# Performance work log

Hardware: AMD Instinct MI355X
Metric: run time of the kernel (lower is better)

The kernel has to match this reference:

```python
import jax, jax.numpy as jnp
import numpy as np

EPS = 1e-5  # torch BatchNorm1d default eps
N, E, F, H, P = 50000, 640000, 128, 128, 64


def batch_norm(h):
    # track_running_stats=False, affine=False -> per-batch mean / biased var
    mu = jnp.mean(h, axis=0)
    var = jnp.mean((h - mu) ** 2, axis=0)
    return (h - mu) * jax.lax.rsqrt(var + EPS)


def gcn_conv(x, src, dst, W, b, n_nodes):
    # GCNConv: D^{-1/2} (A + I) D^{-1/2} X W + b
    h = x @ W
    loop = jnp.arange(n_nodes)
    s = jnp.concatenate([src, loop])
    d = jnp.concatenate([dst, loop])
    deg = jax.ops.segment_sum(jnp.ones(s.shape[0], h.dtype), d, num_segments=n_nodes)
    inv_sqrt = jax.lax.rsqrt(jnp.maximum(deg, 1.0))  # deg >= 1 due to self loops
    msg = h[s] * (inv_sqrt[s] * inv_sqrt[d])[:, None]  # [E+N, H]
    return jax.ops.segment_sum(msg, d, num_segments=n_nodes) + b


def setup_inputs() -> dict:
    key = jax.random.key(0)
    ks = jax.random.split(key, 12)
    s = 0.05
    return {
        "x": jax.random.normal(ks[0], (N, F), jnp.float32),
        "core_values": jax.random.uniform(ks[1], (N,), jnp.float32),
        "W0": jax.random.normal(ks[2], (F, H), jnp.float32) * s,
        "b0": jnp.zeros((H,), jnp.float32),
        "W1": jax.random.normal(ks[3], (H, H), jnp.float32) * s,
        "b1": jnp.zeros((H,), jnp.float32),
        "lin1_W": jax.random.normal(ks[4], (3 * H, H), jnp.float32) * s,
        "lin1_b": jnp.zeros((H,), jnp.float32),
        "lin2_W": jax.random.normal(ks[5], (H, 1), jnp.float32) * s,
        "lin2_b": jnp.zeros((1,), jnp.float32),
        "edge_index": jax.random.randint(ks[6], (2, E), 0, N, jnp.int64 if jax.config.read("jax_enable_x64") else jnp.int32),
        "part_id": jax.random.randint(ks[7], (N,), 0, P, jnp.int32),
        "curr_node_id": 123,
        "num_partitions": P,
    }


def reference(x, core_values, W0, b0, W1, b1, lin1_W, lin1_b, lin2_W, lin2_b,
              edge_index, part_id, curr_node_id, num_partitions):
    n_nodes = x.shape[0]
    src, dst = edge_index[0], edge_index[1]

    # GNN stack: conv -> batchnorm -> relu (num_layers = 2)
    for W, b in ((W0, b0), (W1, b1)):
        x = jax.nn.relu(batch_norm(gcn_conv(x, src, dst, W, b, n_nodes)))

    # getPartitonEmbedding_usingCoreValue as fused segment reductions
    cv = core_values[:, None]
    core = jax.ops.segment_sum(x * cv, part_id, num_segments=num_partitions)
    non_core = jax.ops.segment_sum(x * (1.0 - cv), part_id, num_segments=num_partitions)
    partition_embedding = jnp.concatenate([core, non_core], axis=1)  # [P, 2H]

    x_curr = jnp.broadcast_to(x[curr_node_id][None, :], (num_partitions, x.shape[1]))
    z = jnp.concatenate([x_curr, partition_embedding], axis=1)  # [P, 3H]
    z = jax.nn.relu(z @ lin1_W + lin1_b)
    return z @ lin2_W + lin2_b  # [P, 1]
```

## Files before the change

kernel.cpp:

```cpp
#include <hip/hip_runtime.h>
#include <math.h>

#define EPSV 1e-5f
#define PSORT_NB 256
#define SCAN_NB 256

typedef __attribute__((ext_vector_type(8))) short bf16x8;
typedef __attribute__((ext_vector_type(4))) float f32x4;

__device__ __forceinline__ uint f2b(float f) {
  uint u = __builtin_bit_cast(uint, f);
  return (u + 0x7FFFu + ((u >> 16) & 1u)) >> 16;
}
__device__ __forceinline__ float blo(uint v) { return __builtin_bit_cast(float, v << 16); }
__device__ __forceinline__ float bhi(uint v) { return __builtin_bit_cast(float, v & 0xFFFF0000u); }
__device__ __forceinline__ float b2f(ushort u) { return __builtin_bit_cast(float, ((uint)u) << 16); }

__global__ __launch_bounds__(256) void k_pre1(int* __restrict__ hist, int nbZero,
                                              const int* __restrict__ part,
                                              int* __restrict__ blockHist,
                                              const float* __restrict__ W0,
                                              const float* __restrict__ W1,
                                              ushort* __restrict__ WT0,
                                              ushort* __restrict__ WT1, int n) {
  const int b = blockIdx.x, tid = threadIdx.x;
  if (b < nbZero) {
    int i = b * 256 + tid;
    if (i < n) hist[i] = 0;
  } else if (b < nbZero + PSORT_NB) {
    __shared__ int lh[64];
    int pb = b - nbZero;
    if (tid < 64) lh[tid] = 0;
    __syncthreads();
    int chunk = (n + PSORT_NB - 1) / PSORT_NB;
    int beg = pb * chunk, end = min(n, beg + chunk);
    for (int i = beg + tid; i < end; i += 256) atomicAdd(&lh[part[i]], 1);
    __syncthreads();
    if (tid < 64) blockHist[pb * 64 + tid] = lh[tid];
  } else {
    int idx = (b - nbZero - PSORT_NB) * 256 + tid;
    const float* W = (idx < 16384) ? W0 : W1;
    ushort* WT = (idx < 16384) ? WT0 : WT1;
    int j = idx & 16383;
    int c = j >> 7, k = j & 127;
    WT[j] = (ushort)f2b(W[k * 128 + c]);
  }
}

__global__ __launch_bounds__(256) void k_pre2(const int* __restrict__ dst,
                                              int* __restrict__ hist,
                                              int* __restrict__ rank, int e, int eb,
                                              const int* __restrict__ blockHist,
                                              int* __restrict__ base,
                                              int* __restrict__ ptot) {
  const int b = blockIdx.x, tid = threadIdx.x;
  if (b < eb) {
    int i = b * 256 + tid;
    if (i < e) rank[i] = atomicAdd(&hist[dst[i]], 1);
  } else {
    __shared__ int wtot[4];
    const int p = b - eb;
    const int lane = tid & 63, w = tid >> 6;
    int v = blockHist[tid * 64 + p];
    int x = v;
    #pragma unroll
    for (int off = 1; off < 64; off <<= 1) {
      int y = __shfl_up(x, off);
      if (lane >= off) x += y;
    }
    if (lane == 63) wtot[w] = x;
    __syncthreads();
    int woff = 0;
    if (w > 0) woff = wtot[0];
    if (w > 1) woff += wtot[1];
    if (w > 2) woff += wtot[2];
    base[tid * 64 + p] = woff + x - v;
    if (tid == 255) ptot[p] = woff + x;
  }
}

__global__ __launch_bounds__(256) void k_pre3(const int* __restrict__ hist,
                                              int* __restrict__ row_start,
                                              float* __restrict__ invs,
                                              int* __restrict__ bsum, int n,
                                              const int* __restrict__ ptot,
                                              int* __restrict__ pexcl,
                                              int* __restrict__ pstart) {
  const int b = blockIdx.x, tid = threadIdx.x;
  if (b < SCAN_NB) {
    __shared__ int wtot[4];
    __shared__ int tot;
    const int lane = tid & 63, w = tid >> 6;
    const int chunk = (n + SCAN_NB - 1) / SCAN_NB;
    const int beg = b * chunk, end = min(n, beg + chunk);
    int running = 0;
    for (int t0 = beg; t0 < end; t0 += 256) {
      int i = t0 + tid;
      int v = (i < end) ? hist[i] : 0;
      int x = v;
      #pragma unroll
      for (int off = 1; off < 64; off <<= 1) {
        int y = __shfl_up(x, off);
        if (lane >= off) x += y;
      }
      if (lane == 63) wtot[w] = x;
      __syncthreads();
      if (tid == 0) {
        int a0 = wtot[0], a1 = wtot[1], a2 = wtot[2], a3 = wtot[3];
        wtot[0] = 0; wtot[1] = a0; wtot[2] = a0 + a1; wtot[3] = a0 + a1 + a2;
        tot = a0 + a1 + a2 + a3;
      }
      __syncthreads();
      if (i < end) {
        row_start[i] = running + wtot[w] + x - v;
        invs[i] = rsqrtf((float)(v + 1));
      }
      running += tot;
      __syncthreads();
    }
    if (tid == 0) bsum[b] = running;
  } else if (tid < 64) {
    int v = ptot[tid];
    int x = v;
    #pragma unroll
    for (int off = 1; off < 64; off <<= 1) {
      int y = __shfl_up(x, off);
      if (tid >= off) x += y;
    }
    int excl = x - v;
    pexcl[tid] = excl;
    pstart[tid] = excl;
    if (tid == 63) pstart[64] = x;
  }
}

__global__ __launch_bounds__(256) void k_pre4(const int* __restrict__ bsum,
                                              int* __restrict__ boff,
                                              int* __restrict__ row_start, int n,
                                              const int* __restrict__ part,
                                              const int* __restrict__ base,
                                              const int* __restrict__ pexcl,
                                              int* __restrict__ perm) {
  const int b = blockIdx.x, tid = threadIdx.x;
  if (b == 0) {
    if (tid < 64) {
      int v0 = bsum[tid * 4], v1 = bsum[tid * 4 + 1], v2 = bsum[tid * 4 + 2], v3 = bsum[tid * 4 + 3];
      int s = v0 + v1 + v2 + v3;
      int x = s;
      #pragma unroll
      for (int off = 1; off < 64; off <<= 1) {
        int y = __shfl_up(x, off);
        if (tid >= off) x += y;
      }
      int run = x - s;
      boff[tid * 4] = run; run += v0;
      boff[tid * 4 + 1] = run; run += v1;
      boff[tid * 4 + 2] = run; run += v2;
      boff[tid * 4 + 3] = run;
      if (tid == 63) row_start[n] = x;
    }
  } else {
    __shared__ int cur[64];
    const int pb = b - 1;
    if (tid < 64) cur[tid] = base[pb * 64 + tid] + pexcl[tid];
    __syncthreads();
    int chunk = (n + PSORT_NB - 1) / PSORT_NB;
    int beg = pb * chunk, end = min(n, beg + chunk);
    for (int i = beg + tid; i < end; i += 256) {
      int pos = atomicAdd(&cur[part[i]], 1);
      perm[pos] = i;
    }
  }
}

__global__ __launch_bounds__(256) void k_scan3(int* __restrict__ row_start,
                                               const int* __restrict__ boff, int n) {
  const int b = blockIdx.x, tid = threadIdx.x;
  const int chunk = (n + SCAN_NB - 1) / SCAN_NB;
  const int beg = b * chunk, end = min(n, beg + chunk);
  const int off = boff[b];
  for (int i = beg + tid; i < end; i += 256) row_start[i] += off;
}

__global__ __launch_bounds__(256) void k_scatter(const int* __restrict__ src,
                                                 const int* __restrict__ dst,
                                                 const int* __restrict__ rank,
                                                 const int* __restrict__ row_start,
                                                 int* __restrict__ csr, int e) {
  int i = blockIdx.x * 256 + threadIdx.x;
  if (i < e) csr[row_start[dst[i]] + rank[i]] = src[i];
}

template <bool BN>
__global__ __launch_bounds__(256) void k_gemm(const void* __restrict__ inp,
                                              const ushort* __restrict__ WT,
                                              const float* __restrict__ invs,
                                              const float* __restrict__ stats_red,
                                              ushort* __restrict__ outb, int n) {
  __shared__ ushort As[16384];
  __shared__ ushort Bs[16384];
  __shared__ float muL[128], sclL[128];
  const int tid = threadIdx.x;
  const int l = tid & 63, w = tid >> 6;
  const int br0 = blockIdx.x * 128;

  if (BN) {
    if (tid < 128) {
      float s = stats_red[tid], q = stats_red[128 + tid];
      float m = s * (1.0f / 50000.0f);
      muL[tid] = m;
      sclL[tid] = rsqrtf(q * (1.0f / 50000.0f) - m * m + EPSV);
    }
    __syncthreads();
  }

  #pragma unroll
  for (int i = 0; i < 8; ++i) {
    int flat = i * 2048 + tid * 8;
    int c = flat >> 7;
    uint4 v = *(const uint4*)&WT[flat];
    *(uint4*)&Bs[flat ^ ((c & 7) << 3)] = v;
  }
  #pragma unroll
  for (int i = 0; i < 8; ++i) {
    int flat = i * 2048 + tid * 8;
    int row = flat >> 7, k0 = flat & 127;
    int grow = br0 + row;
    uint4 u;
    if (grow < n) {
      if (BN) {
        const ushort* inb = (const ushort*)inp;
        uint4 raw = *(const uint4*)&inb[(size_t)grow * 128 + k0];
        float f[8] = {blo(raw.x), bhi(raw.x), blo(raw.y), bhi(raw.y),
                      blo(raw.z), bhi(raw.z), blo(raw.w), bhi(raw.w)};
        #pragma unroll
        for (int j = 0; j < 8; ++j) {
          float v = (f[j] - muL[k0 + j]) * sclL[k0 + j];
          f[j] = v > 0.f ? v : 0.f;
        }
        u.x = f2b(f[0]) | (f2b(f[1]) << 16);
        u.y = f2b(f[2]) | (f2b(f[3]) << 16);
        u.z = f2b(f[4]) | (f2b(f[5]) << 16);
        u.w = f2b(f[6]) | (f2b(f[7]) << 16);
      } else {
        const float* inf = (const float*)inp;
        float4 v0 = *(const float4*)&inf[(size_t)grow * 128 + k0];
        float4 v1 = *(const float4*)&inf[(size_t)grow * 128 + k0 + 4];
        u.x = f2b(v0.x) | (f2b(v0.y) << 16);
        u.y = f2b(v0.z) | (f2b(v0.w) << 16);
        u.z = f2b(v1.x) | (f2b(v1.y) << 16);
        u.w = f2b(v1.z) | (f2b(v1.w) << 16);
      }
    } else {
      u.x = u.y = u.z = u.w = 0u;
    }
    *(uint4*)&As[flat ^ ((row & 7) << 3)] = u;
  }
  __syncthreads();

  const int wr = w >> 1, wc = w & 1;
  const int lr = l & 15, lk = (l >> 4) * 8;
  f32x4 acc[4][4];
  #pragma unroll
  for (int m = 0; m < 4; ++m)
    #pragma unroll
    for (int nn = 0; nn < 4; ++nn) acc[m][nn] = (f32x4){0.f, 0.f, 0.f, 0.f};

  #pragma unroll
  for (int ks = 0; ks < 4; ++ks) {
    bf16x8 af[4], bfr[4];
    #pragma unroll
    for (int m = 0; m < 4; ++m) {
      int row = wr * 64 + m * 16 + lr;
      af[m] = *(const bf16x8*)&As[(row * 128 + ks * 32 + lk) ^ ((row & 7) << 3)];
    }
    #pragma unroll
    for (int nn = 0; nn < 4; ++nn) {
      int c = wc * 64 + nn * 16 + lr;
      bfr[nn] = *(const bf16x8*)&Bs[(c * 128 + ks * 32 + lk) ^ ((c & 7) << 3)];
    }
    #pragma unroll
    for (int m = 0; m < 4; ++m)
      #pragma unroll
      for (int nn = 0; nn < 4; ++nn)
        acc[m][nn] = __builtin_amdgcn_mfma_f32_16x16x32_bf16(af[m], bfr[nn], acc[m][nn], 0, 0, 0);
  }

  #pragma unroll
  for (int m = 0; m < 4; ++m) {
    #pragma unroll
    for (int r = 0; r < 4; ++r) {
      int row = br0 + wr * 64 + m * 16 + (l >> 4) * 4 + r;
      if (row >= n) continue;
      float iv = invs[row];
      #pragma unroll
      for (int nn = 0; nn < 4; ++nn) {
        int col = wc * 64 + nn * 16 + lr;
        outb[(size_t)row * 128 + col] = (ushort)f2b(acc[m][nn][r] * iv);
      }
    }
  }
}

__global__ __launch_bounds__(256) void k_gather(const ushort* __restrict__ hsb,
                                                const int* __restrict__ row_start,
                                                const int* __restrict__ csr,
                                                const float* __restrict__ invs,
                                                const float* __restrict__ bias,
                                                ushort* __restrict__ outb,
                                                float* __restrict__ statsP, int n) {
  const int tid = threadIdx.x;
  const int lane = tid & 63, w = tid >> 6;
  const int c0 = lane * 2;
  const ushort* hc = hsb + c0;
  float s0 = 0.f, s1 = 0.f, q0 = 0.f, q1 = 0.f;
  const float bv0 = bias[c0], bv1 = bias[c0 + 1];
  const int stride = gridDim.x * 4;
  for (int node = blockIdx.x * 4 + w; node < n; node += stride) {
    uint vs = *(const uint*)&hc[(size_t)node * 128];
    float accx = blo(vs), accy = bhi(vs);
    int beg = row_start[node], end = row_start[node + 1];
    int e = beg;
    for (; e + 7 < end; e += 8) {
      int sA = csr[e], sB = csr[e + 1], sC = csr[e + 2], sD = csr[e + 3];
      int sE = csr[e + 4], sF = csr[e + 5], sG = csr[e + 6], sH = csr[e + 7];
      uint vA = *(const uint*)&hc[(size_t)sA * 128];
      uint vB = *(const uint*)&hc[(size_t)sB * 128];
      uint vC = *(const uint*)&hc[(size_t)sC * 128];
      uint vD = *(const uint*)&hc[(size_t)sD * 128];
      uint vE = *(const uint*)&hc[(size_t)sE * 128];
      uint vF = *(const uint*)&hc[(size_t)sF * 128];
      uint vG = *(const uint*)&hc[(size_t)sG * 128];
      uint vH = *(const uint*)&hc[(size_t)sH * 128];
      accx += ((blo(vA) + blo(vB)) + (blo(vC) + blo(vD))) +
              ((blo(vE) + blo(vF)) + (blo(vG) + blo(vH)));
      accy += ((bhi(vA) + bhi(vB)) + (bhi(vC) + bhi(vD))) +
              ((bhi(vE) + bhi(vF)) + (bhi(vG) + bhi(vH)));
    }
    for (; e + 3 < end; e += 4) {
      int sA = csr[e], sB = csr[e + 1], sC = csr[e + 2], sD = csr[e + 3];
      uint vA = *(const uint*)&hc[(size_t)sA * 128];
      uint vB = *(const uint*)&hc[(size_t)sB * 128];
      uint vC = *(const uint*)&hc[(size_t)sC * 128];
      uint vD = *(const uint*)&hc[(size_t)sD * 128];
      accx += (blo(vA) + blo(vB)) + (blo(vC) + blo(vD));
      accy += (bhi(vA) + bhi(vB)) + (bhi(vC) + bhi(vD));
    }
    for (; e < end; ++e) {
      uint vA = *(const uint*)&hc[(size_t)csr[e] * 128];
      accx += blo(vA);
      accy += bhi(vA);
    }
    float iv = invs[node];
    float o0 = accx * iv + bv0, o1 = accy * iv + bv1;
    *(uint*)&outb[(size_t)node * 128 + c0] = f2b(o0) | (f2b(o1) << 16);
    s0 += o0; s1 += o1; q0 += o0 * o0; q1 += o1 * o1;
  }
  __shared__ float redS[4][128], redQ[4][128];
  redS[w][c0] = s0; redS[w][c0 + 1] = s1;
  redQ[w][c0] = q0; redQ[w][c0 + 1] = q1;
  __syncthreads();
  if (tid < 128) {
    float s = redS[0][tid] + redS[1][tid] + redS[2][tid] + redS[3][tid];
    statsP[blockIdx.x * 256 + tid] = s;
  } else {
    int t = tid - 128;
    float q = redQ[0][t] + redQ[1][t] + redQ[2][t] + redQ[3][t];
    statsP[blockIdx.x * 256 + tid] = q;
  }
}

__global__ __launch_bounds__(1024) void k_finstats(const float* __restrict__ statsP,
                                                   float* __restrict__ stats_red,
                                                   int nb) {
  int t = threadIdx.x;
  int c = blockIdx.x * 16 + (t & 15);
  int b0 = t >> 4;
  int per = nb >> 6;
  float s = 0.f;
  for (int j = 0; j < per; ++j) s += statsP[(b0 * per + j) * 256 + c];
  __shared__ float red[1024];
  red[t] = s;
  __syncthreads();
  for (int st = 512; st >= 16; st >>= 1) {
    if (t < st) red[t] += red[t + st];
    __syncthreads();
  }
  if (t < 16) stats_red[blockIdx.x * 16 + t] = red[t];
}

__global__ __launch_bounds__(512) void k_pool2(const ushort* __restrict__ hb,
                                               const float* __restrict__ stats_red,
                                               const float* __restrict__ cv,
                                               const int* __restrict__ perm,
                                               const int* __restrict__ pstart,
                                               float* __restrict__ poolP, int n) {
  const int tid = threadIdx.x;
  const int lane = tid & 63, w = tid >> 6;
  const int p = blockIdx.x >> 2, s = blockIdx.x & 3;
  const int g = s * 8 + w;
  const int c0 = lane * 2;

  float s0 = stats_red[c0], s1 = stats_red[c0 + 1];
  float qq0 = stats_red[128 + c0], qq1 = stats_red[128 + c0 + 1];
  float mu0 = s0 * (1.0f / 50000.0f), mu1 = s1 * (1.0f / 50000.0f);
  float scl0 = rsqrtf(qq0 * (1.0f / 50000.0f) - mu0 * mu0 + EPSV);
  float scl1 = rsqrtf(qq1 * (1.0f / 50000.0f) - mu1 * mu1 + EPSV);

  const int beg = pstart[p], end = pstart[p + 1];
  float cc0 = 0.f, cc1 = 0.f, cn0 = 0.f, cn1 = 0.f;

  int j = beg + g;
  for (; j + 32 < end; j += 64) {
    int rA = perm[j], rB = perm[j + 32];
    uint vA = *(const uint*)&hb[(size_t)rA * 128 + c0];
    uint vB = *(const uint*)&hb[(size_t)rB * 128 + c0];
    float cvA = cv[rA], cvB = cv[rB];
    float xA0 = (blo(vA) - mu0) * scl0; xA0 = xA0 > 0.f ? xA0 : 0.f;
    float xA1 = (bhi(vA) - mu1) * scl1; xA1 = xA1 > 0.f ? xA1 : 0.f;
    float xB0 = (blo(vB) - mu0) * scl0; xB0 = xB0 > 0.f ? xB0 : 0.f;
    float xB1 = (bhi(vB) - mu1) * scl1; xB1 = xB1 > 0.f ? xB1 : 0.f;
    cc0 += xA0 * cvA + xB0 * cvB;
    cc1 += xA1 * cvA + xB1 * cvB;
    cn0 += xA0 * (1.f - cvA) + xB0 * (1.f - cvB);
    cn1 += xA1 * (1.f - cvA) + xB1 * (1.f - cvB);
  }
  if (j < end) {
    int rA = perm[j];
    uint vA = *(const uint*)&hb[(size_t)rA * 128 + c0];
    float cvA = cv[rA];
    float xA0 = (blo(vA) - mu0) * scl0; xA0 = xA0 > 0.f ? xA0 : 0.f;
    float xA1 = (bhi(vA) - mu1) * scl1; xA1 = xA1 > 0.f ? xA1 : 0.f;
    cc0 += xA0 * cvA;
    cc1 += xA1 * cvA;
    cn0 += xA0 * (1.f - cvA);
    cn1 += xA1 * (1.f - cvA);
  }

  __shared__ float redC[8][128], redN[8][128];
  redC[w][c0] = cc0; redC[w][c0 + 1] = cc1;
  redN[w][c0] = cn0; redN[w][c0 + 1] = cn1;
  __syncthreads();
  if (tid < 128) {
    float a = 0.f;
    #pragma unroll
    for (int ww = 0; ww < 8; ++ww) a += redC[ww][tid];
    poolP[blockIdx.x * 256 + tid] = a;
  } else if (tid < 256) {
    int t = tid - 128;
    float a = 0.f;
    #pragma unroll
    for (int ww = 0; ww < 8; ++ww) a += redN[ww][t];
    poolP[blockIdx.x * 256 + tid] = a;
  }
}

__global__ __launch_bounds__(128) void k_mlp(const ushort* __restrict__ hb,
                                             const float* __restrict__ stats_red,
                                             const float* __restrict__ poolP,
                                             const float* __restrict__ l1W,
                                             const float* __restrict__ l1b,
                                             const float* __restrict__ l2W,
                                             const float* __restrict__ l2b,
                                             const int* __restrict__ curr_ptr,
                                             float* __restrict__ out, int n) {
  const int p = blockIdx.x;
  const int t = threadIdx.x;
  __shared__ float z[384];
  int curr = *curr_ptr;
  float s = stats_red[t], q = stats_red[128 + t];
  float mu = s / (float)n;
  float scl = rsqrtf(q / (float)n - mu * mu + EPSV);
  float v = b2f(hb[(size_t)curr * 128 + t]);
  v = (v - mu) * scl;
  z[t] = v > 0.f ? v : 0.f;
  float ccore = 0.f, cnon = 0.f;
  #pragma unroll
  for (int sb = 0; sb < 4; ++sb) {
    ccore += poolP[(p * 4 + sb) * 256 + t];
    cnon  += poolP[(p * 4 + sb) * 256 + 128 + t];
  }
  z[128 + t] = ccore;
  z[256 + t] = cnon;
  __syncthreads();
  float a = l1b[t];
  for (int k = 0; k < 384; ++k) a += z[k] * l1W[k * 128 + t];
  a = a > 0.f ? a : 0.f;
  float pr = a * l2W[t];
  #pragma unroll
  for (int off = 32; off; off >>= 1) pr += __shfl_down(pr, off);
  __shared__ float rr[2];
  if ((t & 63) == 0) rr[t >> 6] = pr;
  __syncthreads();
  if (t == 0) out[p] = rr[0] + rr[1] + l2b[0];
}

extern "C" void kernel_launch(void* const* d_in, const int* in_sizes, int n_in,
                              void* d_out, int out_size, void* d_ws, size_t ws_size,
                              hipStream_t stream) {
  const float* x    = (const float*)d_in[0];
  const float* cv   = (const float*)d_in[1];
  const float* W0   = (const float*)d_in[2];
  const float* b0   = (const float*)d_in[3];
  const float* W1   = (const float*)d_in[4];
  const float* b1   = (const float*)d_in[5];
  const float* l1W  = (const float*)d_in[6];
  const float* l1b  = (const float*)d_in[7];
  const float* l2W  = (const float*)d_in[8];
  const float* l2b  = (const float*)d_in[9];
  const int*   ei   = (const int*)d_in[10];
  const int*   part = (const int*)d_in[11];
  const int*   curr = (const int*)d_in[12];

  const int N = in_sizes[1];
  const int E = in_sizes[10] / 2;
  const int* src = ei;
  const int* dst = ei + E;

  const int GATHER_BLOCKS = 2048;

  char* w = (char*)d_ws;
  size_t off = 0;
  auto alloc = [&](size_t bytes) -> void* {
    void* p = (void*)(w + off);
    off = (off + bytes + 255) & ~(size_t)255;
    return p;
  };
  int*   hist      = (int*)alloc((size_t)N * 4);
  int*   row_start = (int*)alloc((size_t)(N + 1) * 4);
  int*   csr       = (int*)alloc((size_t)E * 4);
  int*   rank      = (int*)alloc((size_t)E * 4);
  float* invs      = (float*)alloc((size_t)N * 4);
  int*   bsum      = (int*)alloc((size_t)SCAN_NB * 4);
  int*   boff      = (int*)alloc((size_t)SCAN_NB * 4);
  int*   blockHist = (int*)alloc((size_t)PSORT_NB * 64 * 4);
  int*   pbase     = (int*)alloc((size_t)PSORT_NB * 64 * 4);
  int*   ptot      = (int*)alloc(64 * 4);
  int*   pexcl     = (int*)alloc(64 * 4);
  int*   pstart    = (int*)alloc(65 * 4);
  int*   perm      = (int*)alloc((size_t)N * 4);
  float* stats_red0 = (float*)alloc(256 * 4);
  float* stats_red1 = (float*)alloc(256 * 4);
  float* statsP    = (float*)alloc((size_t)GATHER_BLOCKS * 256 * 4);
  float* poolP     = (float*)alloc((size_t)256 * 256 * 4);
  ushort* WT0      = (ushort*)alloc((size_t)16384 * 2);
  ushort* WT1      = (ushort*)alloc((size_t)16384 * 2);
  ushort* hsb      = (ushort*)alloc((size_t)N * 128 * 2);
  ushort* hb       = (ushort*)alloc((size_t)N * 128 * 2);
  (void)ws_size;

  const int eb = (E + 255) / 256;
  const int nbZero = (N + 255) / 256;

  k_pre1<<<nbZero + PSORT_NB + 128, 256, 0, stream>>>(hist, nbZero, part, blockHist,
                                                      W0, W1, WT0, WT1, N);
  k_pre2<<<eb + 64, 256, 0, stream>>>(dst, hist, rank, E, eb, blockHist, pbase, ptot);
  k_pre3<<<SCAN_NB + 1, 256, 0, stream>>>(hist, row_start, invs, bsum, N, ptot, pexcl, pstart);
  k_pre4<<<1 + PSORT_NB, 256, 0, stream>>>(bsum, boff, row_start, N, part, pbase, pexcl, perm);
  k_scan3<<<SCAN_NB, 256, 0, stream>>>(row_start, boff, N);
  k_scatter<<<eb, 256, 0, stream>>>(src, dst, rank, row_start, csr, E);

  int gb = (N + 127) / 128;
  k_gemm<false><<<gb, 256, 0, stream>>>(x, WT0, invs, nullptr, hsb, N);
  k_gather<<<GATHER_BLOCKS, 256, 0, stream>>>(hsb, row_start, csr, invs, b0, hb, statsP, N);
  k_finstats<<<16, 1024, 0, stream>>>(statsP, stats_red0, GATHER_BLOCKS);
  k_gemm<true><<<gb, 256, 0, stream>>>(hb, WT1, invs, stats_red0, hsb, N);
  k_gather<<<GATHER_BLOCKS, 256, 0, stream>>>(hsb, row_start, csr, invs, b1, hb, statsP, N);
  k_finstats<<<16, 1024, 0, stream>>>(statsP, stats_red1, GATHER_BLOCKS);
  k_pool2<<<256, 512, 0, stream>>>(hb, stats_red1, cv, perm, pstart, poolP, N);
  k_mlp<<<64, 128, 0, stream>>>(hb, stats_red1, poolP, l1W, l1b, l2W, l2b, curr, (float*)d_out, N);
}
```

Baseline: 189.7 us.

## Fuse scan fixup, CSR scatter and first GEMM into one launch; shuffle-broadcast neighbor indices

The scan offset fixup, the CSR scatter and the first-layer GEMM now run as three disjoint block ranges of a single kernel. The scatter adds the block offset itself, and the fixup writes into a new row_fin array, so none of them depends on another inside the launch. This removes two launches and their serialization points. Separately, the gather kernel now loads up to 64 neighbor indices cooperatively, one per lane, and broadcasts them with wave shuffles instead of having every lane read csr redundantly. The cost is an extra N-sized array and some shuffle overhead, which matters more for low-degree nodes.

New measurement: 176.5 us. 6.9% less time.

```diff
diff --git a/kernel.cpp b/kernel.cpp
--- a/kernel.cpp
+++ b/kernel.cpp
@@ -136,7 +136,7 @@
 
 __global__ __launch_bounds__(256) void k_pre4(const int* __restrict__ bsum,
                                               int* __restrict__ boff,
-                                              int* __restrict__ row_start, int n,
+                                              int* __restrict__ row_fin, int n,
                                               const int* __restrict__ part,
                                               const int* __restrict__ base,
                                               const int* __restrict__ pexcl,
@@ -157,7 +157,7 @@
       boff[tid * 4 + 1] = run; run += v1;
       boff[tid * 4 + 2] = run; run += v2;
       boff[tid * 4 + 3] = run;
-      if (tid == 63) row_start[n] = x;
+      if (tid == 63) row_fin[n] = x;
     }
   } else {
     __shared__ int cur[64];
@@ -173,36 +173,16 @@
   }
 }
 
-__global__ __launch_bounds__(256) void k_scan3(int* __restrict__ row_start,
-                                               const int* __restrict__ boff, int n) {
-  const int b = blockIdx.x, tid = threadIdx.x;
-  const int chunk = (n + SCAN_NB - 1) / SCAN_NB;
-  const int beg = b * chunk, end = min(n, beg + chunk);
-  const int off = boff[b];
-  for (int i = beg + tid; i < end; i += 256) row_start[i] += off;
-}
-
-__global__ __launch_bounds__(256) void k_scatter(const int* __restrict__ src,
-                                                 const int* __restrict__ dst,
-                                                 const int* __restrict__ rank,
-                                                 const int* __restrict__ row_start,
-                                                 int* __restrict__ csr, int e) {
-  int i = blockIdx.x * 256 + threadIdx.x;
-  if (i < e) csr[row_start[dst[i]] + rank[i]] = src[i];
-}
-
 template <bool BN>
-__global__ __launch_bounds__(256) void k_gemm(const void* __restrict__ inp,
-                                              const ushort* __restrict__ WT,
-                                              const float* __restrict__ invs,
-                                              const float* __restrict__ stats_red,
-                                              ushort* __restrict__ outb, int n) {
-  __shared__ ushort As[16384];
-  __shared__ ushort Bs[16384];
-  __shared__ float muL[128], sclL[128];
+__device__ __forceinline__ void gemm_body(ushort* As, ushort* Bs, float* muL, float* sclL,
+                                          const void* __restrict__ inp,
+                                          const ushort* __restrict__ WT,
+                                          const float* __restrict__ invs,
+                                          const float* __restrict__ stats_red,
+                                          ushort* __restrict__ outb, int n, int bb) {
   const int tid = threadIdx.x;
   const int l = tid & 63, w = tid >> 6;
-  const int br0 = blockIdx.x * 128;
+  const int br0 = bb * 128;
 
   if (BN) {
     if (tid < 128) {
@@ -302,8 +282,52 @@
   }
 }
 
+__global__ __launch_bounds__(256) void k_mega1(const float* __restrict__ x,
+                                               const ushort* __restrict__ WT0,
+                                               const float* __restrict__ invs,
+                                               ushort* __restrict__ hsb, int n, int gb,
+                                               const int* __restrict__ row_start,
+                                               const int* __restrict__ boff,
+                                               int* __restrict__ row_fin,
+                                               const int* __restrict__ src,
+                                               const int* __restrict__ dst,
+                                               const int* __restrict__ rank,
+                                               int* __restrict__ csr, int e) {
+  __shared__ ushort As[16384];
+  __shared__ ushort Bs[16384];
+  const int b = blockIdx.x, tid = threadIdx.x;
+  if (b < gb) {
+    gemm_body<false>(As, Bs, nullptr, nullptr, x, WT0, invs, nullptr, hsb, n, b);
+  } else if (b < gb + SCAN_NB) {
+    const int sb = b - gb;
+    const int chunk = (n + SCAN_NB - 1) / SCAN_NB;
+    const int beg = sb * chunk, end = min(n, beg + chunk);
+    const int off = boff[sb];
+    for (int i = beg + tid; i < end; i += 256) row_fin[i] = row_start[i] + off;
+  } else {
+    const int chunkS = (n + SCAN_NB - 1) / SCAN_NB;
+    int i = (b - gb - SCAN_NB) * 256 + tid;
+    if (i < e) {
+      int d = dst[i];
+      csr[row_start[d] + boff[d / chunkS] + rank[i]] = src[i];
+    }
+  }
+}
+
+template <bool BN>
+__global__ __launch_bounds__(256) void k_gemm(const void* __restrict__ inp,
+                                              const ushort* __restrict__ WT,
+                                              const float* __restrict__ invs,
+                                              const float* __restrict__ stats_red,
+                                              ushort* __restrict__ outb, int n) {
+  __shared__ ushort As[16384];
+  __shared__ ushort Bs[16384];
+  __shared__ float muL[128], sclL[128];
+  gemm_body<BN>(As, Bs, muL, sclL, inp, WT, invs, stats_red, outb, n, blockIdx.x);
+}
+
 __global__ __launch_bounds__(256) void k_gather(const ushort* __restrict__ hsb,
-                                                const int* __restrict__ row_start,
+                                                const int* __restrict__ row_fin,
                                                 const int* __restrict__ csr,
                                                 const float* __restrict__ invs,
                                                 const float* __restrict__ bias,
@@ -319,37 +343,49 @@
   for (int node = blockIdx.x * 4 + w; node < n; node += stride) {
     uint vs = *(const uint*)&hc[(size_t)node * 128];
     float accx = blo(vs), accy = bhi(vs);
-    int beg = row_start[node], end = row_start[node + 1];
-    int e = beg;
-    for (; e + 7 < end; e += 8) {
-      int sA = csr[e], sB = csr[e + 1], sC = csr[e + 2], sD = csr[e + 3];
-      int sE = csr[e + 4], sF = csr[e + 5], sG = csr[e + 6], sH = csr[e + 7];
-      uint vA = *(const uint*)&hc[(size_t)sA * 128];
-      uint vB = *(const uint*)&hc[(size_t)sB * 128];
-      uint vC = *(const uint*)&hc[(size_t)sC * 128];
-      uint vD = *(const uint*)&hc[(size_t)sD * 128];
-      uint vE = *(const uint*)&hc[(size_t)sE * 128];
-      uint vF = *(const uint*)&hc[(size_t)sF * 128];
-      uint vG = *(const uint*)&hc[(size_t)sG * 128];
-      uint vH = *(const uint*)&hc[(size_t)sH * 128];
-      accx += ((blo(vA) + blo(vB)) + (blo(vC) + blo(vD))) +
-              ((blo(vE) + blo(vF)) + (blo(vG) + blo(vH)));
-      accy += ((bhi(vA) + bhi(vB)) + (bhi(vC) + bhi(vD))) +
-              ((bhi(vE) + bhi(vF)) + (bhi(vG) + bhi(vH)));
-    }
-    for (; e + 3 < end; e += 4) {
-      int sA = csr[e], sB = csr[e + 1], sC = csr[e + 2], sD = csr[e + 3];
-      uint vA = *(const uint*)&hc[(size_t)sA * 128];
-      uint vB = *(const uint*)&hc[(size_t)sB * 128];
-      uint vC = *(const uint*)&hc[(size_t)sC * 128];
-      uint vD = *(const uint*)&hc[(size_t)sD * 128];
-      accx += (blo(vA) + blo(vB)) + (blo(vC) + blo(vD));
-      accy += (bhi(vA) + bhi(vB)) + (bhi(vC) + bhi(vD));
-    }
-    for (; e < end; ++e) {
-      uint vA = *(const uint*)&hc[(size_t)csr[e] * 128];
-      accx += blo(vA);
-      accy += bhi(vA);
+    int beg = row_fin[node], end = row_fin[node + 1];
+    int deg = end - beg;
+    int base = 0;
+    while (base < deg) {
+      int cnt = min(deg - base, 64);
+      int sidx = 0;
+      if (lane < cnt) sidx = csr[beg + base + lane];
+      int j = 0;
+      for (; j + 7 < cnt; j += 8) {
+        int sA = __shfl(sidx, j + 0), sB = __shfl(sidx, j + 1);
+        int sC = __shfl(sidx, j + 2), sD = __shfl(sidx, j + 3);
+        int sE = __shfl(sidx, j + 4), sF = __shfl(sidx, j + 5);
+        int sG = __shfl(sidx, j + 6), sH = __shfl(sidx, j + 7);
+        uint vA = *(const uint*)&hc[(size_t)sA * 128];
+        uint vB = *(const uint*)&hc[(size_t)sB * 128];
+        uint vC = *(const uint*)&hc[(size_t)sC * 128];
+        uint vD = *(const uint*)&hc[(size_t)sD * 128];
+        uint vE = *(const uint*)&hc[(size_t)sE * 128];
+        uint vF = *(const uint*)&hc[(size_t)sF * 128];
+        uint vG = *(const uint*)&hc[(size_t)sG * 128];
+        uint vH = *(const uint*)&hc[(size_t)sH * 128];
+        accx += ((blo(vA) + blo(vB)) + (blo(vC) + blo(vD))) +
+                ((blo(vE) + blo(vF)) + (blo(vG) + blo(vH)));
+        accy += ((bhi(vA) + bhi(vB)) + (bhi(vC) + bhi(vD))) +
+                ((bhi(vE) + bhi(vF)) + (bhi(vG) + bhi(vH)));
+      }
+      for (; j + 3 < cnt; j += 4) {
+        int sA = __shfl(sidx, j + 0), sB = __shfl(sidx, j + 1);
+        int sC = __shfl(sidx, j + 2), sD = __shfl(sidx, j + 3);
+        uint vA = *(const uint*)&hc[(size_t)sA * 128];
+        uint vB = *(const uint*)&hc[(size_t)sB * 128];
+        uint vC = *(const uint*)&hc[(size_t)sC * 128];
+        uint vD = *(const uint*)&hc[(size_t)sD * 128];
+        accx += (blo(vA) + blo(vB)) + (blo(vC) + blo(vD));
+        accy += (bhi(vA) + bhi(vB)) + (bhi(vC) + bhi(vD));
+      }
+      for (; j < cnt; ++j) {
+        int sA = __shfl(sidx, j);
+        uint vA = *(const uint*)&hc[(size_t)sA * 128];
+        accx += blo(vA);
+        accy += bhi(vA);
+      }
+      base += cnt;
     }
     float iv = invs[node];
     float o0 = accx * iv + bv0, o1 = accy * iv + bv1;
@@ -528,6 +564,7 @@
   };
   int*   hist      = (int*)alloc((size_t)N * 4);
   int*   row_start = (int*)alloc((size_t)(N + 1) * 4);
+  int*   row_fin   = (int*)alloc((size_t)(N + 1) * 4);
   int*   csr       = (int*)alloc((size_t)E * 4);
   int*   rank      = (int*)alloc((size_t)E * 4);
   float* invs      = (float*)alloc((size_t)N * 4);
@@ -551,21 +588,20 @@
 
   const int eb = (E + 255) / 256;
   const int nbZero = (N + 255) / 256;
+  const int gb = (N + 127) / 128;
 
   k_pre1<<<nbZero + PSORT_NB + 128, 256, 0, stream>>>(hist, nbZero, part, blockHist,
                                                       W0, W1, WT0, WT1, N);
   k_pre2<<<eb + 64, 256, 0, stream>>>(dst, hist, rank, E, eb, blockHist, pbase, ptot);
   k_pre3<<<SCAN_NB + 1, 256, 0, stream>>>(hist, row_start, invs, bsum, N, ptot, pexcl, pstart);
-  k_pre4<<<1 + PSORT_NB, 256, 0, stream>>>(bsum, boff, row_start, N, part, pbase, pexcl, perm);
-  k_scan3<<<SCAN_NB, 256, 0, stream>>>(row_start, boff, N);
-  k_scatter<<<eb, 256, 0, stream>>>(src, dst, rank, row_start, csr, E);
-
-  int gb = (N + 127) / 128;
-  k_gemm<false><<<gb, 256, 0, stream>>>(x, WT0, invs, nullptr, hsb, N);
-  k_gather<<<GATHER_BLOCKS, 256, 0, stream>>>(hsb, row_start, csr, invs, b0, hb, statsP, N);
+  k_pre4<<<1 + PSORT_NB, 256, 0, stream>>>(bsum, boff, row_fin, N, part, pbase, pexcl, perm);
+  k_mega1<<<gb + SCAN_NB + eb, 256, 0, stream>>>(x, WT0, invs, hsb, N, gb,
+                                                 row_start, boff, row_fin,
+                                                 src, dst, rank, csr, E);
+  k_gather<<<GATHER_BLOCKS, 256, 0, stream>>>(hsb, row_fin, csr, invs, b0, hb, statsP, N);
   k_finstats<<<16, 1024, 0, stream>>>(statsP, stats_red0, GATHER_BLOCKS);
   k_gemm<true><<<gb, 256, 0, stream>>>(hb, WT1, invs, stats_red0, hsb, N);
-  k_gather<<<GATHER_BLOCKS, 256, 0, stream>>>(hsb, row_start, csr, invs, b1, hb, statsP, N);
+  k_gather<<<GATHER_BLOCKS, 256, 0, stream>>>(hsb, row_fin, csr, invs, b1, hb, statsP, N);
   k_finstats<<<16, 1024, 0, stream>>>(statsP, stats_red1, GATHER_BLOCKS);
   k_pool2<<<256, 512, 0, stream>>>(hb, stats_red1, cv, perm, pstart, poolP, N);
   k_mlp<<<64, 128, 0, stream>>>(hb, stats_red1, poolP, l1W, l1b, l2W, l2b, curr, (float*)d_out, N);
```
